# Kernel optimization log

Measured on AMD Instinct MI355X. Metric: run time of the kernel, lower is better.

Reference implementation:

```python
import jax, jax.numpy as jnp
import numpy as np

BN_EPS = 1e-5


def binary_activation(x):
    # ReActNet binary activation: forward = sign(x), backward = d/dx of
    # piecewise polynomial approximation (straight-through estimator).
    out_fwd = jnp.sign(x)
    out3 = jnp.where(x < -1.0, -1.0,
           jnp.where(x < 0.0, x * x + 2.0 * x,
           jnp.where(x < 1.0, -x * x + 2.0 * x, 1.0)))
    return jax.lax.stop_gradient(out_fwd - out3) + out3


def binarize_weights(w):
    # HardBinaryConv: per-output-channel scale = mean(|w|) (detached),
    # binary weight = scale * sign(w), STE through clamp(w, -1, 1).
    scale = jax.lax.stop_gradient(jnp.mean(jnp.abs(w), axis=(1, 2, 3), keepdims=True))
    bw_no_grad = scale * jnp.sign(w)
    cw = jnp.clip(w, -1.0, 1.0)
    return jax.lax.stop_gradient(bw_no_grad - cw) + cw


def setup_inputs() -> dict:
    key = jax.random.key(0)
    k1, k2, k3, k4 = jax.random.split(key, 4)
    x = jax.random.normal(k1, (32, 256, 56, 56), dtype=jnp.float32)
    weight = jax.random.normal(k2, (256, 256, 3, 3), dtype=jnp.float32) * 0.05  # OIHW
    gamma = 1.0 + 0.1 * jax.random.normal(k3, (256,), dtype=jnp.float32)
    beta = 0.1 * jax.random.normal(k4, (256,), dtype=jnp.float32)
    return {"x": x, "weight": weight, "gamma": gamma, "beta": beta}


def reference(x, weight, gamma, beta):
    xa = binary_activation(x)                       # [B, Cin, H, W], values in {-1, 0, +1}
    bw = binarize_weights(weight)                   # [Cout, Cin, 3, 3]
    y = jax.lax.conv_general_dilated(
        xa, bw,
        window_strides=(1, 1),
        padding=((1, 1), (1, 1)),
        dimension_numbers=("NCHW", "OIHW", "NCHW"))  # [B, Cout, H, W]
    # BatchNorm2d, training-mode batch statistics over (N, H, W)
    mean = jnp.mean(y, axis=(0, 2, 3), keepdims=True)
    var = jnp.var(y, axis=(0, 2, 3), keepdims=True)
    yn = (y - mean) * jax.lax.rsqrt(var + BN_EPS)
    y = yn * gamma[None, :, None, None] + beta[None, :, None, None]
    return jax.nn.relu(y)
```

## Files before the change

### kernel.cpp

```cpp
#include <hip/hip_runtime.h>
#include <stdint.h>
#include <type_traits>

#define CIN   256
#define COUT  256
#define HH    56
#define WW    56
#define HW    3136
#define BATCH 32
#define NPIX  (BATCH*HW)
#define PH    58
#define PW    58
#define PPIX  (PH*PW)
#define KTOT  2304
#define BKB   128
#define NKIT  (KTOT/BKB)

typedef int8_t  i8;
typedef int     intx4  __attribute__((ext_vector_type(4)));
typedef int8_t  i8x16  __attribute__((ext_vector_type(16)));
typedef short   short8 __attribute__((ext_vector_type(8)));
typedef float   floatx4 __attribute__((ext_vector_type(4)));

__device__ __forceinline__ void gload_lds16(const i8* g, void* lds_base) {
    __builtin_amdgcn_global_load_lds(
        (const __attribute__((address_space(1))) void*)g,
        (__attribute__((address_space(3))) void*)lds_base,
        16, 0, 0);
}

__global__ __launch_bounds__(256) void prep_w(const float* __restrict__ w,
                                              i8* __restrict__ wg,
                                              float* __restrict__ scale,
                                              float* __restrict__ bnsum,
                                              float* __restrict__ bnsumsq) {
    int o = blockIdx.x;
    int i = threadIdx.x;
    const float* wrow = w + (size_t)o * KTOT + (size_t)i * 9;
    float asum = 0.f;
#pragma unroll
    for (int t = 0; t < 9; ++t) {
        float v = wrow[t];
        asum += fabsf(v);
        wg[(size_t)o * KTOT + t * CIN + i] = (v > 0.f) ? (i8)1 : ((v < 0.f) ? (i8)(-1) : (i8)0);
    }
    for (int off = 32; off > 0; off >>= 1) asum += __shfl_down(asum, off);
    __shared__ float red[4];
    if ((threadIdx.x & 63) == 0) red[threadIdx.x >> 6] = asum;
    __syncthreads();
    if (threadIdx.x == 0) {
        scale[o]   = (red[0] + red[1] + red[2] + red[3]) * (1.f / (float)KTOT);
        bnsum[o]   = 0.f;
        bnsumsq[o] = 0.f;
    }
}

__global__ __launch_bounds__(256) void zero_border(i8* __restrict__ xs) {
    int n  = blockIdx.x / PH;
    int pr = blockIdx.x % PH;
    int* row = (int*)(xs + ((size_t)n * PPIX + (size_t)pr * PW) * CIN);
    if (pr == 0 || pr == PH - 1) {
        for (int idx = threadIdx.x; idx < PW * CIN / 4; idx += 256) row[idx] = 0;
    } else {
        if (threadIdx.x < 64)       row[threadIdx.x] = 0;
        else if (threadIdx.x < 128) row[(PW - 1) * (CIN / 4) + threadIdx.x - 64] = 0;
    }
}

__global__ __launch_bounds__(256) void binarize(const float* __restrict__ x,
                                                i8* __restrict__ xs) {
    __shared__ int lds[64 * 17];
    int p0 = blockIdx.x * 64;
    int c0 = blockIdx.y * 64;
    int n  = blockIdx.z;
    const float* xin = x + (size_t)n * CIN * HW;
    int t   = threadIdx.x;
    int pix = t & 63;
#pragma unroll
    for (int r = 0; r < 4; ++r) {
        int cq = (t >> 6) + 4 * r;
        int packed = 0;
#pragma unroll
        for (int e = 0; e < 4; ++e) {
            float v = xin[(size_t)(c0 + cq * 4 + e) * HW + p0 + pix];
            int s = (v > 0.f) ? 1 : ((v < 0.f) ? -1 : 0);
            packed |= (s & 0xff) << (8 * e);
        }
        lds[pix * 17 + cq] = packed;
    }
    __syncthreads();
    int cch = t & 3;
    int pi  = t >> 2;
    int4 v;
    v.x = lds[pi * 17 + cch * 4 + 0];
    v.y = lds[pi * 17 + cch * 4 + 1];
    v.z = lds[pi * 17 + cch * 4 + 2];
    v.w = lds[pi * 17 + cch * 4 + 3];
    int p = p0 + pi;
    int h = p / WW, w = p - (p / WW) * WW;
    *(int4*)&xs[((size_t)n * PPIX + (size_t)(h + 1) * PW + (w + 1)) * CIN
                + c0 + cch * 16] = v;
}

__global__ __launch_bounds__(256, 2) void conv_gemm(const i8* __restrict__ xs,
                                                    const i8* __restrict__ wg,
                                                    short* __restrict__ y,
                                                    float* __restrict__ bnsum,
                                                    float* __restrict__ bnsumsq) {
    __shared__ __align__(16) i8 smem[65536];

    int tid  = threadIdx.x;
    int lane = tid & 63;
    int wv   = tid >> 6;
    int wm   = wv & 1;
    int wn   = wv >> 1;
    int mt   = blockIdx.x;
    int nt   = blockIdx.y;

    int prow = tid >> 3;
    int koff = ((tid ^ (tid >> 3)) & 7) * 16;
    const i8* aP[4];
    const i8* bP[4];
#pragma unroll
    for (int j = 0; j < 4; ++j) {
        int P = mt * 128 + prow + 32 * j;
        int n = P / HW;
        int p = P - n * HW;
        int h = p / WW;
        int w = p - h * WW;
        aP[j] = xs + ((size_t)n * PPIX + (size_t)h * PW + w) * CIN + koff;
        int o = nt * 128 + prow + 32 * j;
        bP[j] = wg + (size_t)o * KTOT + koff;
    }
    i8* aD[2][4];
    i8* bD[2][4];
#pragma unroll
    for (int b = 0; b < 2; ++b)
#pragma unroll
        for (int j = 0; j < 4; ++j) {
            aD[b][j] = smem + b * 32768 + j * 4096 + wv * 1024;
            bD[b][j] = smem + b * 32768 + 16384 + j * 4096 + wv * 1024;
        }

    int l7  = lane & 7;
    int l15 = lane & 15;
    int lhi = lane >> 4;
    int sw0 = ((lhi ^ l7) << 4);
    int sw1 = sw0 ^ 0x40;
    const i8* Ard0 = smem + (wm * 64 + l15) * BKB + sw0;
    const i8* Ard1 = smem + (wm * 64 + l15) * BKB + sw1;
    const i8* Brd0 = smem + 16384 + (wn * 64 + l15) * BKB + sw0;
    const i8* Brd1 = smem + 16384 + (wn * 64 + l15) * BKB + sw1;

    intx4 acc[4][4];
#pragma unroll
    for (int im = 0; im < 4; ++im)
#pragma unroll
        for (int in = 0; in < 4; ++in) acc[im][in] = intx4{0, 0, 0, 0};

#pragma unroll
    for (int j = 0; j < 4; ++j) gload_lds16(aP[j], aD[0][j]);
#pragma unroll
    for (int j = 0; j < 4; ++j) gload_lds16(bP[j], bD[0][j]);
    __syncthreads();

    auto stage = [&](auto KBC) {
        constexpr int KB  = (int)decltype(KBC)::value;
        constexpr int cur = KB & 1;
        if constexpr (KB < NKIT - 1) {
            constexpr int nb  = KB + 1;
            constexpr int nxt = nb & 1;
            constexpr int ao  = (nb / 6) * PW * CIN + (nb % 6) * 128;
            constexpr int bo  = nb * BKB;
#pragma unroll
            for (int j = 0; j < 4; ++j) gload_lds16(aP[j] + ao, aD[nxt][j]);
#pragma unroll
            for (int j = 0; j < 4; ++j) gload_lds16(bP[j] + bo, bD[nxt][j]);
        }
        constexpr int bufo = cur * 32768;
        intx4 af0[4], bf0[4], af1[4], bf1[4];
#pragma unroll
        for (int im = 0; im < 4; ++im) af0[im] = *(const intx4*)(Ard0 + bufo + im * 2048);
#pragma unroll
        for (int in = 0; in < 4; ++in) bf0[in] = *(const intx4*)(Brd0 + bufo + in * 2048);
#pragma unroll
        for (int im = 0; im < 4; ++im) af1[im] = *(const intx4*)(Ard1 + bufo + im * 2048);
#pragma unroll
        for (int in = 0; in < 4; ++in) bf1[in] = *(const intx4*)(Brd1 + bufo + in * 2048);
#pragma unroll
        for (int im = 0; im < 4; ++im)
#pragma unroll
            for (int in = 0; in < 4; ++in)
                acc[im][in] = __builtin_amdgcn_mfma_i32_16x16x64_i8(
                    af0[im], bf0[in], acc[im][in], 0, 0, 0);
#pragma unroll
        for (int im = 0; im < 4; ++im)
#pragma unroll
            for (int in = 0; in < 4; ++in)
                acc[im][in] = __builtin_amdgcn_mfma_i32_16x16x64_i8(
                    af1[im], bf1[in], acc[im][in], 0, 0, 0);
        __syncthreads();
    };
#define ST(k) stage(std::integral_constant<int, k>{});
    ST(0) ST(1) ST(2) ST(3) ST(4) ST(5) ST(6) ST(7) ST(8)
    ST(9) ST(10) ST(11) ST(12) ST(13) ST(14) ST(15) ST(16) ST(17)
#undef ST

    int colBase = nt * 128 + wn * 64 + l15;
    short* yt = (short*)smem;
#pragma unroll
    for (int in = 0; in < 4; ++in) {
        int o = colBase + in * 16;
        float s1 = 0.f, s2 = 0.f;
#pragma unroll
        for (int im = 0; im < 4; ++im) {
            int r0 = wm * 64 + im * 16 + lhi * 4;
#pragma unroll
            for (int rg = 0; rg < 4; ++rg) {
                int vi = acc[im][in][rg];
                yt[(r0 + rg) * 128 + wn * 64 + in * 16 + l15] = (short)vi;
                float v = (float)vi;
                s1 += v;
                s2 += v * v;
            }
        }
        s1 += __shfl_xor(s1, 16); s2 += __shfl_xor(s2, 16);
        s1 += __shfl_xor(s1, 32); s2 += __shfl_xor(s2, 32);
        if (lhi == 0) {
            atomicAdd(&bnsum[o], s1);
            atomicAdd(&bnsumsq[o], s2);
        }
    }
    __syncthreads();
#pragma unroll
    for (int pass = 0; pass < 8; ++pass) {
        int p = (tid >> 4) + 16 * pass;
        int c = tid & 15;
        *(short8*)&y[(size_t)(mt * 128 + p) * COUT + nt * 128 + c * 8] =
            *(const short8*)&yt[p * 128 + c * 8];
    }
}

__global__ void coeff(const float* __restrict__ bnsum, const float* __restrict__ bnsumsq,
                      const float* __restrict__ scale, const float* __restrict__ gamma,
                      const float* __restrict__ beta, float* __restrict__ kg,
                      float* __restrict__ kc) {
    int o = threadIdx.x;
    float mean = bnsum[o] * (1.f / (float)NPIX);
    float var  = fmaxf(bnsumsq[o] * (1.f / (float)NPIX) - mean * mean, 0.f);
    float sc   = scale[o];
    float inv  = rsqrtf(sc * sc * var + 1e-5f);
    float g    = gamma[o] * sc * inv;
    kg[o] = g;
    kc[o] = beta[o] - mean * g;
}

__global__ __launch_bounds__(256) void bn_out(const short* __restrict__ y,
                                              const float* __restrict__ kg,
                                              const float* __restrict__ kc,
                                              float* __restrict__ out) {
    __shared__ float lds[64 * 65];
    int p0 = blockIdx.x * 64;
    int o0 = blockIdx.y * 64;
    int n  = blockIdx.z;
    int t  = threadIdx.x;
    int cch = t & 7;
    float g[8], c[8];
#pragma unroll
    for (int e = 0; e < 8; ++e) {
        g[e] = kg[o0 + cch * 8 + e];
        c[e] = kc[o0 + cch * 8 + e];
    }
    const short* yb = y + ((size_t)n * HW + p0) * COUT + o0;
#pragma unroll
    for (int j = 0; j < 2; ++j) {
        int pi = (t >> 3) + 32 * j;
        short8 sv = *(const short8*)&yb[(size_t)pi * COUT + cch * 8];
#pragma unroll
        for (int e = 0; e < 8; ++e)
            lds[pi * 65 + cch * 8 + e] = fmaxf(g[e] * (float)sv[e] + c[e], 0.f);
    }
    __syncthreads();
    float* ob = out + ((size_t)n * COUT + o0) * HW + p0;
    int pq = t & 15;
    int ch = t >> 4;
#pragma unroll
    for (int r = 0; r < 4; ++r) {
        int cr = ch + 16 * r;
        floatx4 v;
#pragma unroll
        for (int e = 0; e < 4; ++e) v[e] = lds[(pq * 4 + e) * 65 + cr];
        *(floatx4*)&ob[(size_t)cr * HW + pq * 4] = v;
    }
}

extern "C" void kernel_launch(void* const* d_in, const int* in_sizes, int n_in,
                              void* d_out, int out_size, void* d_ws, size_t ws_size,
                              hipStream_t stream) {
    const float* x     = (const float*)d_in[0];
    const float* w     = (const float*)d_in[1];
    const float* gamma = (const float*)d_in[2];
    const float* beta  = (const float*)d_in[3];
    float* out = (float*)d_out;

    char* ws = (char*)d_ws;
    size_t off = 0;
    i8* xs = (i8*)(ws + off);    off += (size_t)BATCH * PPIX * CIN;
    i8* wg = (i8*)(ws + off);    off += (size_t)COUT * KTOT;
    short* y = (short*)(ws + off); off += (size_t)NPIX * COUT * sizeof(short);
    float* scale   = (float*)(ws + off); off += 1024;
    float* bnsum   = (float*)(ws + off); off += 1024;
    float* bnsumsq = (float*)(ws + off); off += 1024;
    float* kg      = (float*)(ws + off); off += 1024;
    float* kc      = (float*)(ws + off); off += 1024;

    hipLaunchKernelGGL(prep_w, dim3(COUT), dim3(256), 0, stream, w, wg, scale, bnsum, bnsumsq);
    hipLaunchKernelGGL(zero_border, dim3(BATCH * PH), dim3(256), 0, stream, xs);
    hipLaunchKernelGGL(binarize, dim3(HW / 64, CIN / 64, BATCH), dim3(256), 0, stream, x, xs);
    hipLaunchKernelGGL(conv_gemm, dim3(NPIX / 128, 2), dim3(256), 0, stream,
                       xs, wg, y, bnsum, bnsumsq);
    hipLaunchKernelGGL(coeff, dim3(1), dim3(256), 0, stream,
                       bnsum, bnsumsq, scale, gamma, beta, kg, kc);
    hipLaunchKernelGGL(bn_out, dim3(HW / 64, COUT / 64, BATCH), dim3(256), 0, stream,
                       y, kg, kc, out);
}
```

Measured before the change: 307.7 us.

## Prepack weights in MFMA fragment order and load B directly to registers

prep_w now writes binarized weights already arranged in per-lane MFMA B-fragment order, so conv_gemm loads each wave's B operand straight from global memory into registers with double buffering. This drops B from LDS, halving shared memory use and removing the LDS reads for B. The binarize kernel is also rewritten to use vectorized float4 loads without an LDS transpose, at the cost of narrower 4-byte scattered stores. Risks are higher register pressure and global-load latency exposed on the B path.

```diff
diff --git a/kernel.cpp b/kernel.cpp
--- a/kernel.cpp
+++ b/kernel.cpp
@@ -30,19 +30,29 @@
 }
 
 __global__ __launch_bounds__(256) void prep_w(const float* __restrict__ w,
-                                              i8* __restrict__ wg,
+                                              i8* __restrict__ bfr,
                                               float* __restrict__ scale,
                                               float* __restrict__ bnsum,
                                               float* __restrict__ bnsumsq) {
     int o = blockIdx.x;
     int i = threadIdx.x;
     const float* wrow = w + (size_t)o * KTOT + (size_t)i * 9;
+    int seg = o >> 6;
+    int inq = (o >> 4) & 3;
+    int n15 = o & 15;
     float asum = 0.f;
 #pragma unroll
     for (int t = 0; t < 9; ++t) {
         float v = wrow[t];
         asum += fabsf(v);
-        wg[(size_t)o * KTOT + t * CIN + i] = (v > 0.f) ? (i8)1 : ((v < 0.f) ? (i8)(-1) : (i8)0);
+        i8 s = (v > 0.f) ? (i8)1 : ((v < 0.f) ? (i8)(-1) : (i8)0);
+        int k  = t * 256 + i;
+        int kb = k >> 7;
+        int kk = (k >> 6) & 1;
+        int a  = (k >> 4) & 3;
+        int b  = k & 15;
+        int lane = a * 16 + n15;
+        bfr[((((size_t)seg * 18 + kb) * 2 + kk) * 4 + inq) * 1024 + lane * 16 + b] = s;
     }
     for (int off = 32; off > 0; off >>= 1) asum += __shfl_down(asum, off);
     __shared__ float red[4];
@@ -69,45 +79,38 @@
 
 __global__ __launch_bounds__(256) void binarize(const float* __restrict__ x,
                                                 i8* __restrict__ xs) {
-    __shared__ int lds[64 * 17];
     int p0 = blockIdx.x * 64;
     int c0 = blockIdx.y * 64;
     int n  = blockIdx.z;
-    const float* xin = x + (size_t)n * CIN * HW;
-    int t   = threadIdx.x;
-    int pix = t & 63;
-#pragma unroll
-    for (int r = 0; r < 4; ++r) {
-        int cq = (t >> 6) + 4 * r;
-        int packed = 0;
-#pragma unroll
-        for (int e = 0; e < 4; ++e) {
-            float v = xin[(size_t)(c0 + cq * 4 + e) * HW + p0 + pix];
-            int s = (v > 0.f) ? 1 : ((v < 0.f) ? -1 : 0);
-            packed |= (s & 0xff) << (8 * e);
+    int t  = threadIdx.x;
+    int pg = t & 15;
+    int cq = t >> 4;
+    const float* xin = x + (size_t)n * CIN * HW + (size_t)(c0 + 4 * cq) * HW + p0 + 4 * pg;
+    int packed[4] = {0, 0, 0, 0};
+#pragma unroll
+    for (int e = 0; e < 4; ++e) {
+        floatx4 v = *(const floatx4*)(xin + (size_t)e * HW);
+#pragma unroll
+        for (int pp = 0; pp < 4; ++pp) {
+            int s = (v[pp] > 0.f) ? 1 : ((v[pp] < 0.f) ? -1 : 0);
+            packed[pp] |= (s & 0xff) << (8 * e);
         }
-        lds[pix * 17 + cq] = packed;
-    }
-    __syncthreads();
-    int cch = t & 3;
-    int pi  = t >> 2;
-    int4 v;
-    v.x = lds[pi * 17 + cch * 4 + 0];
-    v.y = lds[pi * 17 + cch * 4 + 1];
-    v.z = lds[pi * 17 + cch * 4 + 2];
-    v.w = lds[pi * 17 + cch * 4 + 3];
-    int p = p0 + pi;
-    int h = p / WW, w = p - (p / WW) * WW;
-    *(int4*)&xs[((size_t)n * PPIX + (size_t)(h + 1) * PW + (w + 1)) * CIN
-                + c0 + cch * 16] = v;
+    }
+#pragma unroll
+    for (int pp = 0; pp < 4; ++pp) {
+        int p = p0 + 4 * pg + pp;
+        int h = p / WW, w = p - (p / WW) * WW;
+        *(int*)&xs[((size_t)n * PPIX + (size_t)(h + 1) * PW + (w + 1)) * CIN
+                   + c0 + 4 * cq] = packed[pp];
+    }
 }
 
 __global__ __launch_bounds__(256, 2) void conv_gemm(const i8* __restrict__ xs,
-                                                    const i8* __restrict__ wg,
+                                                    const i8* __restrict__ bfr,
                                                     short* __restrict__ y,
                                                     float* __restrict__ bnsum,
                                                     float* __restrict__ bnsumsq) {
-    __shared__ __align__(16) i8 smem[65536];
+    __shared__ __align__(16) i8 smem[32768];
 
     int tid  = threadIdx.x;
     int lane = tid & 63;
@@ -120,7 +123,6 @@
     int prow = tid >> 3;
     int koff = ((tid ^ (tid >> 3)) & 7) * 16;
     const i8* aP[4];
-    const i8* bP[4];
 #pragma unroll
     for (int j = 0; j < 4; ++j) {
         int P = mt * 128 + prow + 32 * j;
@@ -129,18 +131,13 @@
         int h = p / WW;
         int w = p - h * WW;
         aP[j] = xs + ((size_t)n * PPIX + (size_t)h * PW + w) * CIN + koff;
-        int o = nt * 128 + prow + 32 * j;
-        bP[j] = wg + (size_t)o * KTOT + koff;
     }
     i8* aD[2][4];
-    i8* bD[2][4];
 #pragma unroll
     for (int b = 0; b < 2; ++b)
 #pragma unroll
-        for (int j = 0; j < 4; ++j) {
-            aD[b][j] = smem + b * 32768 + j * 4096 + wv * 1024;
-            bD[b][j] = smem + b * 32768 + 16384 + j * 4096 + wv * 1024;
-        }
+        for (int j = 0; j < 4; ++j)
+            aD[b][j] = smem + b * 16384 + j * 4096 + wv * 1024;
 
     int l7  = lane & 7;
     int l15 = lane & 15;
@@ -149,8 +146,9 @@
     int sw1 = sw0 ^ 0x40;
     const i8* Ard0 = smem + (wm * 64 + l15) * BKB + sw0;
     const i8* Ard1 = smem + (wm * 64 + l15) * BKB + sw1;
-    const i8* Brd0 = smem + 16384 + (wn * 64 + l15) * BKB + sw0;
-    const i8* Brd1 = smem + 16384 + (wn * 64 + l15) * BKB + sw1;
+
+    const i8* bW = bfr + (size_t)(nt * 2 + wn) * 18 * 8192 + lane * 16;
+    intx4 bR[2][8];
 
     intx4 acc[4][4];
 #pragma unroll
@@ -161,7 +159,7 @@
 #pragma unroll
     for (int j = 0; j < 4; ++j) gload_lds16(aP[j], aD[0][j]);
 #pragma unroll
-    for (int j = 0; j < 4; ++j) gload_lds16(bP[j], bD[0][j]);
+    for (int q = 0; q < 8; ++q) bR[0][q] = *(const intx4*)(bW + q * 1024);
     __syncthreads();
 
     auto stage = [&](auto KBC) {
@@ -171,34 +169,30 @@
             constexpr int nb  = KB + 1;
             constexpr int nxt = nb & 1;
             constexpr int ao  = (nb / 6) * PW * CIN + (nb % 6) * 128;
-            constexpr int bo  = nb * BKB;
+#pragma unroll
+            for (int q = 0; q < 8; ++q)
+                bR[nxt][q] = *(const intx4*)(bW + (size_t)nb * 8192 + q * 1024);
 #pragma unroll
             for (int j = 0; j < 4; ++j) gload_lds16(aP[j] + ao, aD[nxt][j]);
-#pragma unroll
-            for (int j = 0; j < 4; ++j) gload_lds16(bP[j] + bo, bD[nxt][j]);
         }
-        constexpr int bufo = cur * 32768;
-        intx4 af0[4], bf0[4], af1[4], bf1[4];
+        constexpr int bufo = cur * 16384;
+        intx4 af0[4], af1[4];
 #pragma unroll
         for (int im = 0; im < 4; ++im) af0[im] = *(const intx4*)(Ard0 + bufo + im * 2048);
 #pragma unroll
-        for (int in = 0; in < 4; ++in) bf0[in] = *(const intx4*)(Brd0 + bufo + in * 2048);
-#pragma unroll
         for (int im = 0; im < 4; ++im) af1[im] = *(const intx4*)(Ard1 + bufo + im * 2048);
-#pragma unroll
-        for (int in = 0; in < 4; ++in) bf1[in] = *(const intx4*)(Brd1 + bufo + in * 2048);
 #pragma unroll
         for (int im = 0; im < 4; ++im)
 #pragma unroll
             for (int in = 0; in < 4; ++in)
                 acc[im][in] = __builtin_amdgcn_mfma_i32_16x16x64_i8(
-                    af0[im], bf0[in], acc[im][in], 0, 0, 0);
+                    af0[im], bR[cur][in], acc[im][in], 0, 0, 0);
 #pragma unroll
         for (int im = 0; im < 4; ++im)
 #pragma unroll
             for (int in = 0; in < 4; ++in)
                 acc[im][in] = __builtin_amdgcn_mfma_i32_16x16x64_i8(
-                    af1[im], bf1[in], acc[im][in], 0, 0, 0);
+                    af1[im], bR[cur][4 + in], acc[im][in], 0, 0, 0);
         __syncthreads();
     };
 #define ST(k) stage(std::integral_constant<int, k>{});
@@ -305,8 +299,8 @@
 
     char* ws = (char*)d_ws;
     size_t off = 0;
-    i8* xs = (i8*)(ws + off);    off += (size_t)BATCH * PPIX * CIN;
-    i8* wg = (i8*)(ws + off);    off += (size_t)COUT * KTOT;
+    i8* xs  = (i8*)(ws + off);    off += (size_t)BATCH * PPIX * CIN;
+    i8* bfr = (i8*)(ws + off);    off += (size_t)COUT * KTOT;
     short* y = (short*)(ws + off); off += (size_t)NPIX * COUT * sizeof(short);
     float* scale   = (float*)(ws + off); off += 1024;
     float* bnsum   = (float*)(ws + off); off += 1024;
@@ -314,11 +308,11 @@
     float* kg      = (float*)(ws + off); off += 1024;
     float* kc      = (float*)(ws + off); off += 1024;
 
-    hipLaunchKernelGGL(prep_w, dim3(COUT), dim3(256), 0, stream, w, wg, scale, bnsum, bnsumsq);
+    hipLaunchKernelGGL(prep_w, dim3(COUT), dim3(256), 0, stream, w, bfr, scale, bnsum, bnsumsq);
     hipLaunchKernelGGL(zero_border, dim3(BATCH * PH), dim3(256), 0, stream, xs);
     hipLaunchKernelGGL(binarize, dim3(HW / 64, CIN / 64, BATCH), dim3(256), 0, stream, x, xs);
     hipLaunchKernelGGL(conv_gemm, dim3(NPIX / 128, 2), dim3(256), 0, stream,
-                       xs, wg, y, bnsum, bnsumsq);
+                       xs, bfr, y, bnsum, bnsumsq);
     hipLaunchKernelGGL(coeff, dim3(1), dim3(256), 0, stream,
                        bnsum, bnsumsq, scale, gamma, beta, kg, kc);
     hipLaunchKernelGGL(bn_out, dim3(HW / 64, COUT / 64, BATCH), dim3(256), 0, stream,
```

Result: slower. 317.6 us (+3.2%).
